# Kernel tuning notes

Measured on AMD Instinct MI355X. Metric: run time of the kernel, lower is better.

## Reference

```python
import jax, jax.numpy as jnp
import numpy as np
from jax import lax

B, C, H, W = 8, 256, 32, 32
HEADS = 8
NUM_OFF = 9
OFF_SCALE = 0.1


def setup_inputs() -> dict:
    key = jax.random.key(0)
    ks = jax.random.split(key, 8)
    f = lambda k, s, sc: jax.random.normal(k, s, dtype=jnp.float32) * sc
    return {
        'query_map': f(ks[0], (B, C, H, W), 1.0),
        'kv_map': f(ks[1], (B, C, H, W), 1.0),
        'Wq': f(ks[2], (C, C), C ** -0.5),
        'Wk': f(ks[3], (C, C), C ** -0.5),
        'Wv': f(ks[4], (C, C), C ** -0.5),
        'Woff1': f(ks[5], (C // 2, C, 3, 3), (C * 9) ** -0.5),
        'boff1': jnp.zeros((C // 2,), jnp.float32),
        'Woff2': f(ks[6], (NUM_OFF * 2, C // 2), (C // 2) ** -0.5),
        'boff2': jnp.zeros((NUM_OFF * 2,), jnp.float32),
        'Wout': f(ks[7], (C, C), C ** -0.5),
        'bout': jnp.zeros((C,), jnp.float32),
    }


def grid_sample_bilinear_border(img, grid):
    """img: (B,C,H,W); grid: (B,H,W,2) with (x,y) in [-1,1], align_corners=True,
    padding_mode='border'. Returns (B,C,H,W)."""
    Bn, Cn, Hn, Wn = img.shape
    x = (grid[..., 0] + 1.0) * 0.5 * (Wn - 1)
    y = (grid[..., 1] + 1.0) * 0.5 * (Hn - 1)
    # border padding: clamp continuous coords into the valid range
    x = jnp.clip(x, 0.0, Wn - 1)
    y = jnp.clip(y, 0.0, Hn - 1)
    x0 = jnp.floor(x)
    y0 = jnp.floor(y)
    wx = x - x0
    wy = y - y0
    x0i = x0.astype(jnp.int32)
    y0i = y0.astype(jnp.int32)
    x1i = jnp.minimum(x0i + 1, Wn - 1)
    y1i = jnp.minimum(y0i + 1, Hn - 1)
    flat = img.reshape(Bn, Cn, Hn * Wn)

    def gat(iy, ix):
        idx = (iy * Wn + ix).reshape(Bn, 1, -1)  # broadcasts over channels
        return jnp.take_along_axis(flat, idx, axis=2)

    v00 = gat(y0i, x0i)
    v01 = gat(y0i, x1i)
    v10 = gat(y1i, x0i)
    v11 = gat(y1i, x1i)
    wxf = wx.reshape(Bn, 1, -1)
    wyf = wy.reshape(Bn, 1, -1)
    out = (v00 * (1 - wxf) + v01 * wxf) * (1 - wyf) + (v10 * (1 - wxf) + v11 * wxf) * wyf
    return out.reshape(Bn, Cn, Hn, Wn)


def reference(query_map, kv_map, Wq, Wk, Wv, Woff1, boff1, Woff2, boff2, Wout, bout):
    Bn, Cn, Hn, Wn = query_map.shape
    hd = Cn // HEADS
    # 1x1 conv projections as channel einsums
    q = jnp.einsum('oc,bchw->bohw', Wq, query_map)
    # offset network: 3x3 conv -> relu -> 1x1 conv
    h1 = lax.conv_general_dilated(q, Woff1, (1, 1), 'SAME',
                                  dimension_numbers=('NCHW', 'OIHW', 'NCHW'))
    h1 = jax.nn.relu(h1 + boff1[None, :, None, None])
    offsets = jnp.einsum('oc,bchw->bohw', Woff2, h1) + boff2[None, :, None, None]
    offsets = offsets.reshape(Bn, NUM_OFF, 2, Hn, Wn)
    offset = offsets[:, 0] * OFF_SCALE  # (B,2,H,W); ch0 -> x, ch1 -> y
    # normalized base grid in [-1,1] (align_corners=True convention)
    gx = jnp.linspace(-1.0, 1.0, Wn, dtype=q.dtype)[None, :]  # (1,W)
    gy = jnp.linspace(-1.0, 1.0, Hn, dtype=q.dtype)[:, None]  # (H,1)
    vx = gx[None] + offset[:, 0]  # (B,H,W)
    vy = gy[None] + offset[:, 1]
    vgrid = jnp.stack([vx, vy], axis=-1)  # (B,H,W,2)
    kv_sampled = grid_sample_bilinear_border(kv_map, vgrid)
    k = jnp.einsum('oc,bchw->bohw', Wk, kv_sampled)
    v = jnp.einsum('oc,bchw->bohw', Wv, kv_sampled)
    # (B,C,H,W) -> (B,heads,HW,hd)
    def to_heads(t):
        return t.reshape(Bn, HEADS, hd, Hn * Wn).transpose(0, 1, 3, 2)
    qh, kh, vh = to_heads(q), to_heads(k), to_heads(v)
    scale = hd ** -0.5
    attn = jnp.einsum('bhqd,bhkd->bhqk', qh, kh) * scale
    attn = jax.nn.softmax(attn, axis=-1)
    out = jnp.einsum('bhqk,bhkd->bhqd', attn, vh)
    out = out.transpose(0, 1, 3, 2).reshape(Bn, Cn, Hn, Wn)
    out = jnp.einsum('oc,bchw->bohw', Wout, out) + bout[None, :, None, None]
    return out
```

## Files before the change

### kernel.cpp

```cpp
#include <hip/hip_runtime.h>

#define HW_ 1024

typedef __attribute__((ext_vector_type(8))) short bf16x8;
typedef __attribute__((ext_vector_type(4))) short bf16x4;
typedef __attribute__((ext_vector_type(4))) float f32x4;

__device__ inline unsigned short f2bf(float f) {
  unsigned int u = __float_as_uint(f);
  u += 0x7FFF + ((u >> 16) & 1);
  return (unsigned short)(u >> 16);
}
__device__ inline unsigned short f2bf_fast(float f) {
  return (unsigned short)((__float_as_uint(f) + 0x8000u) >> 16);
}
__device__ inline float bf2f(unsigned short h) {
  return __uint_as_float(((unsigned int)h) << 16);
}
__device__ inline void async_copy16(const void* g, void* l) {
  __builtin_amdgcn_global_load_lds(
      (const __attribute__((address_space(1))) unsigned int*)g,
      (__attribute__((address_space(3))) unsigned int*)l, 16, 0, 0);
}

__global__ __launch_bounds__(256) void fused0(
    const float* __restrict__ kv,
    const float* __restrict__ Wq, const float* __restrict__ Wk,
    const float* __restrict__ Wv, const float* __restrict__ Wo,
    const float* __restrict__ Woff1, const float* __restrict__ Xf,
    short* __restrict__ WH, short* __restrict__ WL, short* __restrict__ wb,
    float* __restrict__ kvT,
    short* __restrict__ Yt, short* __restrict__ Yh2, short* __restrict__ Yl2)
{
  __shared__ float T[256][33];
  __shared__ short Bsh[32][40];
  __shared__ short Bsl[32][40];
  const int bid = blockIdx.x, t = threadIdx.x;

  if (bid < 512) {
    const int w    = t >> 6;
    const int lane = t & 63;
    const int ln   = lane & 15;
    const int qd   = lane >> 4;
    const int bp0  = (bid & 255) * 32;
    const int om   = (bid >> 8) * 128 + w * 32;
    const int bB   = bp0 >> 10, p0l = bp0 & 1023;

    f32x4 acc[2][2] = {};
#pragma unroll
    for (int k0 = 0; k0 < 256; k0 += 32) {
      __syncthreads();
      {
        int pp = t & 31, cg = t >> 5;
        float fv[4];
#pragma unroll
        for (int j = 0; j < 4; ++j)
          fv[j] = Xf[((size_t)(bB * 256 + k0 + cg * 4 + j)) * HW_ + p0l + pp];
        bf16x4 h4, l4;
#pragma unroll
        for (int j = 0; j < 4; ++j) {
          unsigned short h = f2bf(fv[j]);
          h4[j] = (short)h;
          l4[j] = (short)f2bf(fv[j] - bf2f(h));
        }
        *(bf16x4*)&Bsh[pp][cg * 4] = h4;
        *(bf16x4*)&Bsl[pp][cg * 4] = l4;
      }
      __syncthreads();

      bf16x8 Ah[2], Al[2], Bh[2], Bl[2];
#pragma unroll
      for (int mt = 0; mt < 2; ++mt) {
        const float* ws = &Wq[((size_t)(om + mt * 16 + ln)) * 256 + k0 + qd * 8];
        float4 fa = *(const float4*)ws;
        float4 fb = *(const float4*)(ws + 4);
        float f8[8] = {fa.x, fa.y, fa.z, fa.w, fb.x, fb.y, fb.z, fb.w};
#pragma unroll
        for (int j = 0; j < 8; ++j) {
          unsigned short h = f2bf(f8[j]);
          Ah[mt][j] = (short)h;
          Al[mt][j] = (short)f2bf(f8[j] - bf2f(h));
        }
      }
#pragma unroll
      for (int nt = 0; nt < 2; ++nt) {
        Bh[nt] = *(const bf16x8*)&Bsh[nt * 16 + ln][qd * 8];
        Bl[nt] = *(const bf16x8*)&Bsl[nt * 16 + ln][qd * 8];
      }
#pragma unroll
      for (int mt = 0; mt < 2; ++mt)
#pragma unroll
        for (int nt = 0; nt < 2; ++nt) {
          acc[mt][nt] = __builtin_amdgcn_mfma_f32_16x16x32_bf16(Ah[mt], Bh[nt], acc[mt][nt], 0, 0, 0);
          acc[mt][nt] = __builtin_amdgcn_mfma_f32_16x16x32_bf16(Ah[mt], Bl[nt], acc[mt][nt], 0, 0, 0);
          acc[mt][nt] = __builtin_amdgcn_mfma_f32_16x16x32_bf16(Al[mt], Bh[nt], acc[mt][nt], 0, 0, 0);
        }
    }

    const float sc = 0.25506063286f;
#pragma unroll
    for (int mt = 0; mt < 2; ++mt)
#pragma unroll
      for (int nt = 0; nt < 2; ++nt) {
        int bp = bp0 + nt * 16 + ln;
        int b = bp >> 10, p = bp & 1023;
#pragma unroll
        for (int i = 0; i < 4; ++i) {
          int o = om + mt * 16 + qd * 4 + i;
          int h = o >> 5, d = o & 31;
          Yt[(((size_t)(b * 8 + h)) * 1024 + p) * 32 + d] = (short)f2bf(acc[mt][nt][i] * sc);
        }
        int ob = om + mt * 16 + qd * 4;
        bf16x4 h4, l4;
#pragma unroll
        for (int i = 0; i < 4; ++i) {
          float f = acc[mt][nt][i];
          unsigned short h = f2bf(f);
          h4[i] = (short)h;
          l4[i] = (short)f2bf(f - bf2f(h));
        }
        *(bf16x4*)&Yh2[(size_t)bp * 256 + ob] = h4;
        *(bf16x4*)&Yl2[(size_t)bp * 256 + ob] = l4;
      }

  } else if (bid < 768) {
    int tb = bid - 512;
    int b = tb >> 5, p0 = (tb & 31) * 32;
    int pp = t & 31, cg = t >> 5;
#pragma unroll
    for (int i = 0; i < 32; ++i) {
      int c = cg * 32 + i;
      T[c][pp] = kv[((size_t)(b * 256 + c)) * HW_ + p0 + pp];
    }
    __syncthreads();
#pragma unroll
    for (int r = 0; r < 8; ++r) {
      int e = t + 256 * r;
      int c4 = (e & 63) * 4, pp2 = e >> 6;
      float4 v4;
      v4.x = T[c4 + 0][pp2];
      v4.y = T[c4 + 1][pp2];
      v4.z = T[c4 + 2][pp2];
      v4.w = T[c4 + 3][pp2];
      *(float4*)&kvT[((size_t)(b * 1024 + p0 + pp2)) * 256 + c4] = v4;
    }
  } else if (bid < 960) {
    int b2 = bid - 768;
    int mat = b2 >> 6;
    int loc = (b2 & 63) * 1024 + t * 4;
    const float* W = (mat == 0) ? Wk : (mat == 1) ? Wv : Wo;
    float4 f4 = *(const float4*)&W[loc];
    float f[4] = {f4.x, f4.y, f4.z, f4.w};
    bf16x4 h4, l4;
#pragma unroll
    for (int j = 0; j < 4; ++j) {
      unsigned short h = f2bf(f[j]);
      h4[j] = (short)h;
      l4[j] = (short)f2bf(f[j] - bf2f(h));
    }
    *(bf16x4*)&WH[(mat + 1) * 65536 + loc] = h4;
    *(bf16x4*)&WL[(mat + 1) * 65536 + loc] = l4;
  } else {
    int e0 = (bid - 960) * 1024 + t * 4;
#pragma unroll
    for (int j = 0; j < 4; ++j) {
      int e = e0 + j;
      int c = e & 255;
      int o = (e >> 8) & 127;
      int tap = e >> 15;
      wb[e] = (short)f2bf(Woff1[((size_t)(o * 256 + c)) * 9 + tap]);
    }
  }
}

__global__ __launch_bounds__(512) void convkv(
    const short* __restrict__ wb, const float* __restrict__ bias,
    const float* __restrict__ W2, const float* __restrict__ b2,
    const short* __restrict__ xh, const short* __restrict__ xl,
    const float* __restrict__ kvT,
    const short* __restrict__ WH, const short* __restrict__ WL,
    short* __restrict__ kt, short* __restrict__ vt)
{
  __shared__ short Xs[2][3][34][264];
  __shared__ short XsH[32][264];
  __shared__ short XsL[32][264];
  __shared__ float red[4][32][2];
  __shared__ float2 crd[32];
  const int id   = blockIdx.x;
  const int b    = id & 7;
  const int y0   = id >> 3;
  const int t    = threadIdx.x;
  const int w    = t >> 6;
  const int lane = t & 63;
  const int ln   = lane & 15;
  const int qd   = lane >> 4;
  const int bp0  = (b * 32 + y0) * 32;

  {
    bf16x8 v[12];
#pragma unroll
    for (int i = 0; i < 12; ++i) {
      int e = t + 512 * i;
      int oct = e & 31;
      int x   = (e >> 5) & 31;
      int rr  = e >> 10;
      int hl  = rr / 3, r = rr % 3;
      int yy  = y0 + r - 1;
      bf16x8 val = {};
      if (yy >= 0 && yy < 32) {
        const short* src = hl ? xl : xh;
        val = *(const bf16x8*)&src[((size_t)((b * 32 + yy) * 32 + x)) * 256 + oct * 8];
      }
      v[i] = val;
    }
#pragma unroll
    for (int i = 0; i < 12; ++i) {
      int e = t + 512 * i;
      int oct = e & 31;
      int x   = (e >> 5) & 31;
      int rr  = e >> 10;
      int hl  = rr / 3, r = rr % 3;
      *(bf16x8*)&Xs[hl][r][x + 1][oct * 8] = v[i];
    }
    if (t < 384) {
      int oct  = t & 31;
      int colw = (t >> 5) & 1;
      int rr   = t >> 6;
      int hl   = rr / 3, r = rr % 3;
      bf16x8 zz = {};
      *(bf16x8*)&Xs[hl][r][colw ? 33 : 0][oct * 8] = zz;
    }
  }
  __syncthreads();

  const int chh = w >> 2;
  const int ow  = w & 3;
  const int o0c = ow * 32;
  f32x4 acc[2][2] = {};
#pragma unroll
  for (int c0s = 0; c0s < 4; ++c0s) {
    const int c0 = chh * 128 + c0s * 32;
#pragma unroll
    for (int tap = 0; tap < 9; ++tap) {
      const int ky = tap / 3, kx = tap % 3;
      bf16x8 afr[2];
#pragma unroll
      for (int m = 0; m < 2; ++m)
        afr[m] = *(const bf16x8*)&wb[((size_t)(tap * 128 + o0c + m * 16 + ln)) * 256
                                     + c0 + qd * 8];
#pragma unroll
      for (int nt = 0; nt < 2; ++nt) {
        int hc = nt * 16 + ln + kx;
        bf16x8 bh = *(const bf16x8*)&Xs[0][ky][hc][c0 + qd * 8];
        bf16x8 bl = *(const bf16x8*)&Xs[1][ky][hc][c0 + qd * 8];
#pragma unroll
        for (int m = 0; m < 2; ++m) {
          acc[m][nt] = __builtin_amdgcn_mfma_f32_16x16x32_bf16(afr[m], bh, acc[m][nt], 0, 0, 0);
          acc[m][nt] = __builtin_amdgcn_mfma_f32_16x16x32_bf16(afr[m], bl, acc[m][nt], 0, 0, 0);
        }
      }
    }
  }

  float* ps = (float*)&XsH[0][0];
  if (w >= 4) {
#pragma unroll
    for (int m = 0; m < 2; ++m)
#pragma unroll
      for (int nt = 0; nt < 2; ++nt)
        *(f32x4*)&ps[(((w - 4) * 64 + lane) * 4 + m * 2 + nt) * 4] = acc[m][nt];
  }
  __syncthreads();

  if (w < 4) {
    float ps0[2] = {0.f, 0.f}, ps1[2] = {0.f, 0.f};
#pragma unroll
    for (int m = 0; m < 2; ++m)
#pragma unroll
      for (int nt = 0; nt < 2; ++nt) {
        f32x4 p = *(const f32x4*)&ps[((w * 64 + lane) * 4 + m * 2 + nt) * 4];
        acc[m][nt] += p;
      }
#pragma unroll
    for (int m = 0; m < 2; ++m)
#pragma unroll
      for (int i = 0; i < 4; ++i) {
        int o = o0c + m * 16 + qd * 4 + i;
        float bo = bias[o];
        float w2a = W2[o], w2b = W2[128 + o];
#pragma unroll
        for (int nt = 0; nt < 2; ++nt) {
          float h = fmaxf(acc[m][nt][i] + bo, 0.f);
          ps0[nt] += w2a * h;
          ps1[nt] += w2b * h;
        }
      }
#pragma unroll
    for (int msk = 16; msk < 64; msk <<= 1) {
      ps0[0] += __shfl_xor(ps0[0], msk, 64);
      ps0[1] += __shfl_xor(ps0[1], msk, 64);
      ps1[0] += __shfl_xor(ps1[0], msk, 64);
      ps1[1] += __shfl_xor(ps1[1], msk, 64);
    }
    if (qd == 0) {
#pragma unroll
      for (int nt = 0; nt < 2; ++nt) {
        red[w][nt * 16 + ln][0] = ps0[nt];
        red[w][nt * 16 + ln][1] = ps1[nt];
      }
    }
  }
  __syncthreads();
  if (t < 32) {
    float c0s = (red[0][t][0] + red[1][t][0]) + (red[2][t][0] + red[3][t][0]) + b2[0];
    float c1s = (red[0][t][1] + red[1][t][1]) + (red[2][t][1] + red[3][t][1]) + b2[1];
    float gx = -1.f + 2.f * (float)t / 31.f;
    float gy = -1.f + 2.f * (float)y0 / 31.f;
    float vx = gx + 0.1f * c0s;
    float vy = gy + 0.1f * c1s;
    float px = fminf(fmaxf((vx + 1.f) * 0.5f * 31.f, 0.f), 31.f);
    float py = fminf(fmaxf((vy + 1.f) * 0.5f * 31.f, 0.f), 31.f);
    crd[t] = make_float2(px, py);
  }
  __syncthreads();

#pragma unroll
  for (int it = 0; it < 2; ++it) {
    int e = t + 512 * it;
    int oct = e & 31, row = e >> 5;
    float2 cd = crd[row];
    float x0f = floorf(cd.x), y0f = floorf(cd.y);
    float wx = cd.x - x0f, wy = cd.y - y0f;
    int x0 = (int)x0f, y0i = (int)y0f;
    int x1 = min(x0 + 1, 31), y1 = min(y0i + 1, 31);
    float w00 = (1.f - wx) * (1.f - wy), w01 = wx * (1.f - wy);
    float w10 = (1.f - wx) * wy,         w11 = wx * wy;
    const float* r00 = &kvT[((size_t)(b * 1024 + y0i * 32 + x0)) * 256 + oct * 8];
    const float* r01 = &kvT[((size_t)(b * 1024 + y0i * 32 + x1)) * 256 + oct * 8];
    const float* r10 = &kvT[((size_t)(b * 1024 + y1 * 32 + x0)) * 256 + oct * 8];
    const float* r11 = &kvT[((size_t)(b * 1024 + y1 * 32 + x1)) * 256 + oct * 8];
    float4 a00 = *(const float4*)r00, b00 = *(const float4*)(r00 + 4);
    float4 a01 = *(const float4*)r01, b01 = *(const float4*)(r01 + 4);
    float4 a10 = *(const float4*)r10, b10 = *(const float4*)(r10 + 4);
    float4 a11 = *(const float4*)r11, b11 = *(const float4*)(r11 + 4);
    float v[8];
    v[0] = a00.x * w00 + a01.x * w01 + a10.x * w10 + a11.x * w11;
    v[1] = a00.y * w00 + a01.y * w01 + a10.y * w10 + a11.y * w11;
    v[2] = a00.z * w00 + a01.z * w01 + a10.z * w10 + a11.z * w11;
    v[3] = a00.w * w00 + a01.w * w01 + a10.w * w10 + a11.w * w11;
    v[4] = b00.x * w00 + b01.x * w01 + b10.x * w10 + b11.x * w11;
    v[5] = b00.y * w00 + b01.y * w01 + b10.y * w10 + b11.y * w11;
    v[6] = b00.z * w00 + b01.z * w01 + b10.z * w10 + b11.z * w11;
    v[7] = b00.w * w00 + b01.w * w01 + b10.w * w10 + b11.w * w11;
    bf16x8 h8, l8;
#pragma unroll
    for (int j = 0; j < 8; ++j) {
      unsigned short h = f2bf(v[j]);
      h8[j] = (short)h;
      l8[j] = (short)f2bf(v[j] - bf2f(h));
    }
    *(bf16x8*)&XsH[row][oct * 8] = h8;
    *(bf16x8*)&XsL[row][oct * 8] = l8;
  }
  __syncthreads();

  const int mat  = w >> 2;
  const short* WAh = WH + (mat ? 131072 : 65536);
  const short* WAl = WL + (mat ? 131072 : 65536);
  const int om = (w & 3) * 64;

  f32x4 acg[4][2] = {};
#pragma unroll
  for (int k0 = 0; k0 < 256; k0 += 32) {
    bf16x8 Bh[2], Bl[2];
#pragma unroll
    for (int nt = 0; nt < 2; ++nt) {
      Bh[nt] = *(const bf16x8*)&XsH[nt * 16 + ln][k0 + qd * 8];
      Bl[nt] = *(const bf16x8*)&XsL[nt * 16 + ln][k0 + qd * 8];
    }
#pragma unroll
    for (int mt = 0; mt < 4; ++mt) {
      size_t wi = ((size_t)(om + mt * 16 + ln)) * 256 + k0 + qd * 8;
      bf16x8 Ah = *(const bf16x8*)&WAh[wi];
      bf16x8 Al = *(const bf16x8*)&WAl[wi];
#pragma unroll
      for (int nt = 0; nt < 2; ++nt) {
        acg[mt][nt] = __builtin_amdgcn_mfma_f32_16x16x32_bf16(Ah, Bh[nt], acg[mt][nt], 0, 0, 0);
        acg[mt][nt] = __builtin_amdgcn_mfma_f32_16x16x32_bf16(Ah, Bl[nt], acg[mt][nt], 0, 0, 0);
        acg[mt][nt] = __builtin_amdgcn_mfma_f32_16x16x32_bf16(Al, Bh[nt], acg[mt][nt], 0, 0, 0);
      }
    }
  }

#pragma unroll
  for (int mt = 0; mt < 4; ++mt)
#pragma unroll
    for (int nt = 0; nt < 2; ++nt) {
      int p  = bp0 + nt * 16 + ln;
      int pl = p & 1023;
      int jt = pl >> 6, jl = pl & 63;
#pragma unroll
      for (int i = 0; i < 4; ++i) {
        int oc = om + mt * 16 + qd * 4 + i;
        unsigned short val = f2bf(acg[mt][nt][i]);
        int bhead = b * 8 + (oc >> 5), d = oc & 31;
        if (mat == 0) {
          int cd2 = (d >> 3) ^ ((jl >> 2) & 3);
          kt[((((size_t)(bhead * 16 + jt)) * 64 + jl) * 4 + cd2) * 8 + (d & 7)] = (short)val;
        } else {
          int jjs = ((jl & 15) << 2) | (jl >> 4);
          int cj = (jjs >> 3) ^ (d & 7);
          vt[((((size_t)(bhead * 16 + jt)) * 32 + d) * 8 + cj) * 8 + (jjs & 7)] = (short)val;
        }
      }
    }
}

__global__ __launch_bounds__(256) void attn_mfma(
    const short* __restrict__ qt, const short* __restrict__ kt,
    const short* __restrict__ vt, short* __restrict__ aoh,
    short* __restrict__ aol)
{
  __shared__ __align__(16) short Ks[2][2048];
  __shared__ __align__(16) short Vs[2][2048];
  __shared__ __align__(16) short P[4][32][72];
  const int t    = threadIdx.x;
  const int w    = t >> 6;
  const int lane = t & 63;
  const int ln   = lane & 15;
  const int qd   = lane >> 4;
  const int id   = blockIdx.x;
  const int b    = id & 7;
  const int rem  = id >> 3;
  const int h    = rem & 7;
  const int qc   = rem >> 3;
  const int bh   = b * 8 + h;
  const int qbase = qc * 128 + w * 16;

  const short* ktb = kt + (size_t)bh * 32768;
  const short* vtb = vt + (size_t)bh * 32768;

  bf16x8 aq[2];
  aq[0] = *(const bf16x8*)&qt[((size_t)(bh * 1024 + qbase + ln)) * 32 + qd * 8];
  aq[1] = *(const bf16x8*)&qt[((size_t)(bh * 1024 + qbase + 64 + ln)) * 32 + qd * 8];

  f32x4 acc[2][2] = {};
  float lacc[2][4] = {};
  const f32x4 zero = {0.f, 0.f, 0.f, 0.f};

  const int stoff = w * 512 + lane * 8;
  const int ldoff = w * 512;

  async_copy16(&ktb[stoff], &Ks[0][ldoff]);
  async_copy16(&vtb[stoff], &Vs[0][ldoff]);
  __syncthreads();

  for (int jt = 0; jt < 16; ++jt) {
    const int cur = jt & 1, nxt = cur ^ 1;
    if (jt < 15) {
      async_copy16(&ktb[(jt + 1) * 2048 + stoff], &Ks[nxt][ldoff]);
      async_copy16(&vtb[(jt + 1) * 2048 + stoff], &Vs[nxt][ldoff]);
    }

    bf16x8 bk[4], bv[2][2];
#pragma unroll
    for (int kk = 0; kk < 4; ++kk)
      bk[kk] = *(const bf16x8*)&Ks[cur][((kk * 16 + ln) * 4 + (qd ^ ((ln >> 2) & 3))) * 8];
#pragma unroll
    for (int kc = 0; kc < 2; ++kc)
#pragma unroll
      for (int ds = 0; ds < 2; ++ds)
        bv[kc][ds] = *(const bf16x8*)&Vs[cur][((ds * 16 + ln) * 8 + ((kc * 4 + qd) ^ (ln & 7))) * 8];

#pragma unroll
    for (int qf = 0; qf < 2; ++qf) {
      f32x4 s[4];
      __builtin_amdgcn_s_setprio(1);
#pragma unroll
      for (int kk = 0; kk < 4; ++kk)
        s[kk] = __builtin_amdgcn_mfma_f32_16x16x32_bf16(aq[qf], bk[kk], zero, 0, 0, 0);
      __builtin_amdgcn_s_setprio(0);

#pragma unroll
      for (int i = 0; i < 4; ++i) {
        float p0 = __builtin_amdgcn_exp2f(s[0][i]);
        float p1 = __builtin_amdgcn_exp2f(s[1][i]);
        float p2 = __builtin_amdgcn_exp2f(s[2][i]);
        float p3 = __builtin_amdgcn_exp2f(s[3][i]);
        s[0][i] = p0; s[1][i] = p1; s[2][i] = p2; s[3][i] = p3;
        lacc[qf][i] += (p0 + p1) + (p2 + p3);
      }
#pragma unroll
      for (int i = 0; i < 4; ++i) {
        bf16x4 p4;
#pragma unroll
        for (int kk = 0; kk < 4; ++kk) p4[kk] = (short)f2bf_fast(s[kk][i]);
        *(bf16x4*)&P[w][qf * 16 + qd * 4 + i][4 * ln] = p4;
      }
      __builtin_amdgcn_s_setprio(1);
#pragma unroll
      for (int kc = 0; kc < 2; ++kc) {
        bf16x8 ap = *(const bf16x8*)&P[w][qf * 16 + ln][kc * 32 + qd * 8];
#pragma unroll
        for (int ds = 0; ds < 2; ++ds)
          acc[qf][ds] = __builtin_amdgcn_mfma_f32_16x16x32_bf16(ap, bv[kc][ds], acc[qf][ds], 0, 0, 0);
      }
      __builtin_amdgcn_s_setprio(0);
    }

    __syncthreads();
  }

  const int bb = bh >> 3, hh2 = bh & 7;
#pragma unroll
  for (int qf = 0; qf < 2; ++qf)
#pragma unroll
    for (int i = 0; i < 4; ++i) {
      float l = lacc[qf][i];
      l += __shfl_xor(l, 1, 64);
      l += __shfl_xor(l, 2, 64);
      l += __shfl_xor(l, 4, 64);
      l += __shfl_xor(l, 8, 64);
      float inv = 1.f / l;
      int qrow = qbase + qf * 64 + qd * 4 + i;
#pragma unroll
      for (int ds = 0; ds < 2; ++ds) {
        float v = acc[qf][ds][i] * inv;
        unsigned short hv = f2bf(v);
        size_t idx = ((size_t)(bb * 1024 + qrow)) * 256 + hh2 * 32 + ds * 16 + ln;
        aoh[idx] = (short)hv;
        aol[idx] = (short)f2bf(v - bf2f(hv));
      }
    }
}

__global__ __launch_bounds__(256) void gemm_out(
    const short* __restrict__ Wh, const short* __restrict__ Wl,
    const short* __restrict__ Xh, const short* __restrict__ Xl,
    const float* __restrict__ bias, float* __restrict__ Yf)
{
  const int t    = threadIdx.x;
  const int w    = t >> 6;
  const int lane = t & 63;
  const int ln   = lane & 15;
  const int qd   = lane >> 4;
  const int bp0  = blockIdx.x * 32;
  const int om   = blockIdx.y * 128 + w * 32;

  f32x4 acc[2][2] = {};
#pragma unroll
  for (int k0 = 0; k0 < 256; k0 += 32) {
    bf16x8 Ah[2], Al[2], Bh[2], Bl[2];
#pragma unroll
    for (int mt = 0; mt < 2; ++mt) {
      size_t wi = ((size_t)(om + mt * 16 + ln)) * 256 + k0 + qd * 8;
      Ah[mt] = *(const bf16x8*)&Wh[wi];
      Al[mt] = *(const bf16x8*)&Wl[wi];
    }
#pragma unroll
    for (int nt = 0; nt < 2; ++nt) {
      size_t xi = ((size_t)(bp0 + nt * 16 + ln)) * 256 + k0 + qd * 8;
      Bh[nt] = *(const bf16x8*)&Xh[xi];
      Bl[nt] = *(const bf16x8*)&Xl[xi];
    }
#pragma unroll
    for (int mt = 0; mt < 2; ++mt)
#pragma unroll
      for (int nt = 0; nt < 2; ++nt) {
        acc[mt][nt] = __builtin_amdgcn_mfma_f32_16x16x32_bf16(Ah[mt], Bh[nt], acc[mt][nt], 0, 0, 0);
        acc[mt][nt] = __builtin_amdgcn_mfma_f32_16x16x32_bf16(Ah[mt], Bl[nt], acc[mt][nt], 0, 0, 0);
        acc[mt][nt] = __builtin_amdgcn_mfma_f32_16x16x32_bf16(Al[mt], Bh[nt], acc[mt][nt], 0, 0, 0);
      }
  }

#pragma unroll
  for (int mt = 0; mt < 2; ++mt)
#pragma unroll
    for (int i = 0; i < 4; ++i) {
      int o = om + mt * 16 + qd * 4 + i;
      float bo = bias[o];
#pragma unroll
      for (int nt = 0; nt < 2; ++nt) {
        int bp = bp0 + nt * 16 + ln;
        int b = bp >> 10, p = bp & 1023;
        Yf[((size_t)(b * 256 + o)) * HW_ + p] = acc[mt][nt][i] + bo;
      }
    }
}

extern "C" void kernel_launch(void* const* d_in, const int* in_sizes, int n_in,
                              void* d_out, int out_size, void* d_ws, size_t ws_size,
                              hipStream_t stream)
{
  const float* query_map = (const float*)d_in[0];
  const float* kv_map    = (const float*)d_in[1];
  const float* Wq        = (const float*)d_in[2];
  const float* Wk        = (const float*)d_in[3];
  const float* Wv        = (const float*)d_in[4];
  const float* Woff1     = (const float*)d_in[5];
  const float* boff1     = (const float*)d_in[6];
  const float* Woff2     = (const float*)d_in[7];
  const float* boff2     = (const float*)d_in[8];
  const float* Wout      = (const float*)d_in[9];
  const float* bout      = (const float*)d_in[10];
  float* out = (float*)d_out;
  char* base = (char*)d_ws;

  const size_t MB = 1u << 20;
  short* qt     = (short*)(base + 1 * MB);
  short* kt     = (short*)(base + 5 * MB);
  short* vt     = (short*)(base + 9 * MB);
  short* bufBh  = (short*)(base + 13 * MB);
  short* bufBl  = (short*)(base + 17 * MB);
  short* wb     = (short*)(base + 21 * MB);
  short* WH     = (short*)(base + 22 * MB);
  short* WL     = (short*)(base + 23 * MB);
  float* kvT    = (float*)(base + 24 * MB);

  fused0<<<dim3(1248), dim3(256), 0, stream>>>(kv_map, Wq, Wk, Wv, Wout, Woff1,
                                               query_map, WH, WL, wb, kvT,
                                               qt, bufBh, bufBl);
  convkv<<<dim3(256), dim3(512), 0, stream>>>(wb, boff1, Woff2, boff2,
                                              bufBh, bufBl, kvT, WH, WL, kt, vt);
  attn_mfma<<<dim3(512), dim3(256), 0, stream>>>(qt, kt, vt, bufBh, bufBl);
  gemm_out<<<dim3(256, 2), dim3(256), 0, stream>>>(WH + 196608, WL + 196608,
                                                   bufBh, bufBl, bout, out);
}
```

Baseline: 179.5 us.

## Pre-swizzle conv and K/V weights into MFMA fragment order for coalesced loads

The prep kernel now writes the 3x3 offset-conv weights and the Wk/Wv bf16 hi/lo splits in a tiled layout where each lane's 8-element MFMA A-fragment sits contiguously, with lanes adjacent in memory. The conv and K/V projection loops index this layout directly, so every wavefront fetches one contiguous 1 KB block instead of 16-byte pieces strided by 512 bytes. The Woff1 conversion also now emits vectorized 4-element stores. The aim is lower global/L2 traffic and fewer partial cache-line accesses on weight fetches. The risk is that the prep layout and the consumer indexing must stay in exact agreement.

Result: faster. 171.0 us (-4.7%).

```diff
diff --git a/kernel.cpp b/kernel.cpp
--- a/kernel.cpp
+++ b/kernel.cpp
@@ -158,18 +158,30 @@
       h4[j] = (short)h;
       l4[j] = (short)f2bf(f[j] - bf2f(h));
     }
-    *(bf16x4*)&WH[(mat + 1) * 65536 + loc] = h4;
-    *(bf16x4*)&WL[(mat + 1) * 65536 + loc] = l4;
+    if (mat == 2) {
+      *(bf16x4*)&WH[3 * 65536 + loc] = h4;
+      *(bf16x4*)&WL[3 * 65536 + loc] = l4;
+    } else {
+      int r = loc >> 8, c = loc & 255;
+      int mtile = r >> 4, k0s = c >> 5;
+      int lane_ = ((c >> 3) & 3) * 16 + (r & 15);
+      int pidx = (((mtile * 8 + k0s) * 64 + lane_) * 8) + (c & 7);
+      *(bf16x4*)&WH[(mat + 1) * 65536 + pidx] = h4;
+      *(bf16x4*)&WL[(mat + 1) * 65536 + pidx] = l4;
+    }
   } else {
     int e0 = (bid - 960) * 1024 + t * 4;
-#pragma unroll
-    for (int j = 0; j < 4; ++j) {
-      int e = e0 + j;
-      int c = e & 255;
-      int o = (e >> 8) & 127;
-      int tap = e >> 15;
-      wb[e] = (short)f2bf(Woff1[((size_t)(o * 256 + c)) * 9 + tap]);
-    }
+    int c = e0 & 255;
+    int o = (e0 >> 8) & 127;
+    int tap = e0 >> 15;
+    bf16x4 h4;
+#pragma unroll
+    for (int j = 0; j < 4; ++j)
+      h4[j] = (short)f2bf(Woff1[((size_t)(o * 256 + c + j)) * 9 + tap]);
+    int otile = o >> 4, c0s = c >> 5;
+    int lane_ = ((c >> 3) & 3) * 16 + (o & 15);
+    int widx = ((((tap * 8 + otile) * 8 + c0s) * 64 + lane_) * 8) + (c & 7);
+    *(bf16x4*)&wb[widx] = h4;
   }
 }
 
@@ -240,14 +252,15 @@
 #pragma unroll
   for (int c0s = 0; c0s < 4; ++c0s) {
     const int c0 = chh * 128 + c0s * 32;
+    const int c0abs = chh * 4 + c0s;
 #pragma unroll
     for (int tap = 0; tap < 9; ++tap) {
       const int ky = tap / 3, kx = tap % 3;
       bf16x8 afr[2];
 #pragma unroll
       for (int m = 0; m < 2; ++m)
-        afr[m] = *(const bf16x8*)&wb[((size_t)(tap * 128 + o0c + m * 16 + ln)) * 256
-                                     + c0 + qd * 8];
+        afr[m] = *(const bf16x8*)&wb[((((tap * 8 + (ow * 2 + m)) * 8 + c0abs) * 64
+                                       + lane) * 8)];
 #pragma unroll
       for (int nt = 0; nt < 2; ++nt) {
         int hc = nt * 16 + ln + kx;
@@ -367,11 +380,12 @@
   const int mat  = w >> 2;
   const short* WAh = WH + (mat ? 131072 : 65536);
   const short* WAl = WL + (mat ? 131072 : 65536);
-  const int om = (w & 3) * 64;
+  const int om4 = (w & 3) * 4;
 
   f32x4 acg[4][2] = {};
 #pragma unroll
   for (int k0 = 0; k0 < 256; k0 += 32) {
+    const int k0s = k0 >> 5;
     bf16x8 Bh[2], Bl[2];
 #pragma unroll
     for (int nt = 0; nt < 2; ++nt) {
@@ -380,7 +394,7 @@
     }
 #pragma unroll
     for (int mt = 0; mt < 4; ++mt) {
-      size_t wi = ((size_t)(om + mt * 16 + ln)) * 256 + k0 + qd * 8;
+      size_t wi = ((size_t)(((om4 + mt) * 8 + k0s) * 64 + lane)) * 8;
       bf16x8 Ah = *(const bf16x8*)&WAh[wi];
       bf16x8 Al = *(const bf16x8*)&WAl[wi];
 #pragma unroll
@@ -401,7 +415,7 @@
       int jt = pl >> 6, jl = pl & 63;
 #pragma unroll
       for (int i = 0; i < 4; ++i) {
-        int oc = om + mt * 16 + qd * 4 + i;
+        int oc = (w & 3) * 64 + mt * 16 + qd * 4 + i;
         unsigned short val = f2bf(acg[mt][nt][i]);
         int bhead = b * 8 + (oc >> 5), d = oc & 31;
         if (mat == 0) {
```
